# Kernel optimization log

Measured on AMD Instinct MI355X. Metric: run time of the kernel, lower is better.

## Reference

```python
import jax, jax.numpy as jnp
import numpy as np

D_IN = 4096
FEATURES = 4096
BATCH = 4096
NUM_ACTIVE = 50
ACTIVE_VAL = 3.0


def _sparse_init(key, shape, num_active=NUM_ACTIVE, active_val=ACTIVE_VAL):
    # Per output column: num_active inputs start ON (active_val), rest OFF (-3.0)
    scores = jax.random.uniform(key, shape)
    k = min(num_active, shape[0])
    threshold = jnp.sort(scores, axis=0)[-k]
    return jnp.where(scores >= threshold[None, :], active_val, -3.0).astype(jnp.float32)


def setup_inputs() -> dict:
    key = jax.random.key(0)
    kx, kw = jax.random.split(key)
    x = jax.random.normal(kx, (BATCH, D_IN), dtype=jnp.float32)
    w_raw = _sparse_init(kw, (D_IN, FEATURES))
    return {"x": x, "w_raw": w_raw}


def reference(x, w_raw):
    # Binary weights via straight-through estimator.
    w_soft = jax.nn.sigmoid(w_raw)
    w_hard = (w_raw > 0.0).astype(jnp.float32)
    w = w_soft + jax.lax.stop_gradient(w_hard - w_soft)
    return x @ w
```

## Files before the change

### kernel.cpp

```cpp
#include <hip/hip_runtime.h>
#include <hip/hip_fp16.h>

#define D_IN 4096
#define FEAT 4096
#define BATCH 4096
#define MAX_SLOTS 64
#define BFEAT 16
#define RCAP 8
#define OVCAP 16

typedef _Float16 h2 __attribute__((ext_vector_type(2)));

__device__ __forceinline__ h2 bc(unsigned u) { return __builtin_bit_cast(h2, u); }

__global__ void scan_kernel(const float* __restrict__ w,
                            unsigned int* __restrict__ c16,
                            unsigned char* __restrict__ rbuf,
                            unsigned int* __restrict__ ocnt,
                            unsigned short* __restrict__ ovf) {
    int t = blockIdx.x * blockDim.x + threadIdx.x;
    float4 v = ((const float4*)w)[t];
    int flat = t * 4;
    float a[4] = {v.x, v.y, v.z, v.w};
#pragma unroll
    for (int c = 0; c < 4; ++c) {
        if (a[c] > 0.0f) {
            int e = flat + c;
            int F = e & (FEAT - 1);
            int i = e >> 12;
            int r = i & 15;
            unsigned int p = atomicAdd(&c16[(F << 4) + r], 1u);
            if (p < RCAP) {
                rbuf[(size_t)((F << 4) + r) * RCAP + p] = (unsigned char)(i >> 4);
            } else {
                unsigned int op = atomicAdd(&ocnt[F], 1u);
                if (op < OVCAP) ovf[(size_t)F * OVCAP + op] = (unsigned short)i;
            }
        }
    }
}

__global__ __launch_bounds__(256)
void emit_kernel(const unsigned int* __restrict__ c16,
                 const unsigned char* __restrict__ rbuf,
                 const unsigned int* __restrict__ ocnt,
                 const unsigned short* __restrict__ ovf,
                 unsigned int* __restrict__ cnt,
                 unsigned short* __restrict__ idx) {
    __shared__ __align__(16) unsigned short outl[BFEAT][MAX_SLOTS];
    __shared__ unsigned short extras[BFEAT][48];
    __shared__ unsigned char  gapsl[BFEAT][48];
    __shared__ int            scnt[BFEAT][16];
    __shared__ unsigned char  kk[BFEAT][16];
    __shared__ unsigned char  mm[BFEAT][16];
    __shared__ unsigned int   ecnt[BFEAT], gcnt[BFEAT];
    __shared__ unsigned short nn[BFEAT];

    const int tid = threadIdx.x;
    const int f0  = blockIdx.x * BFEAT;
    const int f   = tid >> 4, r = tid & 15;
    const int F   = f0 + f;

    if (tid < BFEAT) { ecnt[tid] = 0u; gcnt[tid] = 0u; }
    ((unsigned int*)outl)[tid] = 0u;
    ((unsigned int*)outl)[tid + 256] = 0u;

    {
        unsigned int c = c16[(F << 4) + r];
        int kr = c > RCAP ? RCAP : (int)c;
        kk[f][r] = (unsigned char)kr;
        scnt[f][r] = kr;
    }
    __syncthreads();

    if (r == 0) {
        int s = 0;
#pragma unroll
        for (int q = 0; q < 16; ++q) s += (int)kk[f][q];
        int ov = (int)ocnt[F]; if (ov > OVCAP) ov = OVCAP;
        s += ov;
        if (s > MAX_SLOTS) s = MAX_SLOTS;
        nn[f] = (unsigned short)s;
        cnt[F] = (unsigned int)s;
    }
    __syncthreads();

    {
        const int n  = (int)nn[f];
        const int kr = (int)kk[f][r];
        uint2 braw = *reinterpret_cast<const uint2*>(rbuf + (size_t)((F << 4) + r) * RCAP);
        const unsigned char* bs = reinterpret_cast<const unsigned char*>(&braw);
        const int base = (r - F) & 15;
        const int tgt  = (n >> 4) + (base < (n & 15) ? 1 : 0);
        const int m    = kr < tgt ? kr : tgt;
        mm[f][r] = (unsigned char)m;
        for (int j = 0; j < m; ++j)
            outl[f][base + (j << 4)] = (unsigned short)(((int)bs[j] << 8) | (r << 4));
    }
    __syncthreads();

    if (tid < MAX_SLOTS) {
        const int p = tid;
        const int j = p >> 4;
        unsigned used = 0u;
        unsigned gapf = 0u;
#pragma unroll
        for (int ff = 0; ff < BFEAT; ++ff) {
            if (p < (int)nn[ff]) {
                const int rr = (p + f0 + ff) & 15;
                if (j < (int)mm[ff][rr]) used |= 1u << rr;
                else                     gapf |= 1u << ff;
            }
        }
        while (gapf) {
            const int ff = __builtin_ctz(gapf);
            gapf &= gapf - 1;
            const int rr = (p + f0 + ff) & 15;
            int got = -1, gr = -1;
            for (int dr = 1; dr < 16; ++dr) {
                const int rc = (rr + dr) & 15;
                if ((used >> rc) & 1u) continue;
                const int t = atomicSub(&scnt[ff][rc], 1) - 1;
                if (t >= (int)mm[ff][rc]) { got = t; gr = rc; break; }
            }
            if (got >= 0) {
                const unsigned char item =
                    rbuf[(size_t)(((f0 + ff) << 4) + gr) * RCAP + got];
                outl[ff][p] = (unsigned short)(((int)item << 8) | (gr << 4));
                used |= 1u << gr;
            } else {
                unsigned int g = atomicAdd(&gcnt[ff], 1u);
                if (g < 48) gapsl[ff][g] = (unsigned char)p;
            }
        }
    }
    __syncthreads();

    {
        const int lo = (int)mm[f][r];
        int hi = scnt[f][r];
        const int kr = (int)kk[f][r];
        if (hi > kr) hi = kr;
        for (int t = lo; t < hi; ++t) {
            unsigned int e = atomicAdd(&ecnt[f], 1u);
            if (e < 48) {
                const unsigned char item = rbuf[(size_t)((F << 4) + r) * RCAP + t];
                extras[f][e] = (unsigned short)(((int)item << 8) | (r << 4));
            }
        }
    }
    if (r == 0) {
        int ov = (int)ocnt[F]; if (ov > OVCAP) ov = OVCAP;
        for (int jj = 0; jj < ov; ++jj) {
            unsigned int e = atomicAdd(&ecnt[f], 1u);
            if (e < 48) extras[f][e] = (unsigned short)(ovf[(size_t)F * OVCAP + jj] << 4);
        }
    }
    __syncthreads();

    if (tid < BFEAT) {
        const int ff = tid;
        int g = (int)gcnt[ff]; if (g > 48) g = 48;
        int e = (int)ecnt[ff]; if (e > 48) e = 48;
        const int m2 = g < e ? g : e;
        for (int t = 0; t < m2; ++t)
            outl[ff][gapsl[ff][t]] = extras[ff][t];
    }
    __syncthreads();

    if (tid < BFEAT * 8) {
        const int ff = tid >> 3, o = tid & 7;
        const uint4 v = *reinterpret_cast<const uint4*>(&outl[ff][o << 3]);
        reinterpret_cast<uint4*>(idx)[(size_t)o * FEAT + f0 + ff] = v;
    }
}

__device__ __forceinline__ void do_oct(uint4 p, const char* __restrict__ xtb,
                                       h2& A01, h2& A23, h2& A45, h2& A67,
                                       h2& B01, h2& B23, h2& B45, h2& B67) {
    uint4 v0 = *(const uint4*)(xtb + (p.x & 0xFFF0u));
    uint4 v1 = *(const uint4*)(xtb + (p.x >> 16));
    uint4 v2 = *(const uint4*)(xtb + (p.y & 0xFFF0u));
    uint4 v3 = *(const uint4*)(xtb + (p.y >> 16));
    uint4 v4 = *(const uint4*)(xtb + (p.z & 0xFFF0u));
    uint4 v5 = *(const uint4*)(xtb + (p.z >> 16));
    uint4 v6 = *(const uint4*)(xtb + (p.w & 0xFFF0u));
    uint4 v7 = *(const uint4*)(xtb + (p.w >> 16));
    A01 += bc(v0.x); A23 += bc(v0.y); A45 += bc(v0.z); A67 += bc(v0.w);
    B01 += bc(v1.x); B23 += bc(v1.y); B45 += bc(v1.z); B67 += bc(v1.w);
    A01 += bc(v2.x); A23 += bc(v2.y); A45 += bc(v2.z); A67 += bc(v2.w);
    B01 += bc(v3.x); B23 += bc(v3.y); B45 += bc(v3.z); B67 += bc(v3.w);
    A01 += bc(v4.x); A23 += bc(v4.y); A45 += bc(v4.z); A67 += bc(v4.w);
    B01 += bc(v5.x); B23 += bc(v5.y); B45 += bc(v5.z); B67 += bc(v5.w);
    A01 += bc(v6.x); A23 += bc(v6.y); A45 += bc(v6.z); A67 += bc(v6.w);
    B01 += bc(v7.x); B23 += bc(v7.y); B45 += bc(v7.z); B67 += bc(v7.w);
}

__global__ __launch_bounds__(1024, 8)
void gather_kernel(const float* __restrict__ x,
                   const unsigned int* __restrict__ cnt,
                   const uint4* __restrict__ q,
                   const unsigned short* __restrict__ q16,
                   float* __restrict__ out) {
    __shared__ uint4 xt[D_IN];
    const int tid = threadIdx.x;
    const int b0  = blockIdx.x * 8;
    const float* xb = x + (size_t)b0 * D_IN;

    {
        const int c4 = tid << 2;
        float4 r0 = *(const float4*)(xb + c4);
        float4 r1 = *(const float4*)(xb + c4 + D_IN);
        float4 r2 = *(const float4*)(xb + c4 + 2 * D_IN);
        float4 r3 = *(const float4*)(xb + c4 + 3 * D_IN);
        float4 r4 = *(const float4*)(xb + c4 + 4 * D_IN);
        float4 r5 = *(const float4*)(xb + c4 + 5 * D_IN);
        float4 r6 = *(const float4*)(xb + c4 + 6 * D_IN);
        float4 r7 = *(const float4*)(xb + c4 + 7 * D_IN);
#define PACK_COL(cc, comp)                                          \
        {                                                           \
            __half2 p01 = __floats2half2_rn(r0.comp, r1.comp);      \
            __half2 p23 = __floats2half2_rn(r2.comp, r3.comp);      \
            __half2 p45 = __floats2half2_rn(r4.comp, r5.comp);      \
            __half2 p67 = __floats2half2_rn(r6.comp, r7.comp);      \
            uint4 v;                                                \
            v.x = *(unsigned*)&p01;                                 \
            v.y = *(unsigned*)&p23;                                 \
            v.z = *(unsigned*)&p45;                                 \
            v.w = *(unsigned*)&p67;                                 \
            xt[c4 + cc] = v;                                        \
        }
        PACK_COL(0, x) PACK_COL(1, y) PACK_COL(2, z) PACK_COL(3, w)
#undef PACK_COL
    }
    __syncthreads();

    const char* xtb = (const char*)xt;

#pragma unroll
    for (int k = 0; k < 4; k += 2) {
        const int fA = tid + k * 1024;
        const int fB = fA + 1024;
        int nA = (int)cnt[fA]; if (nA > MAX_SLOTS) nA = MAX_SLOTS;
        int nB = (int)cnt[fB]; if (nB > MAX_SLOTS) nB = MAX_SLOTS;
        const uint4* qA = q + fA;
        const uint4* qB = q + fB;

        h2 aA01 = {0,0}, aA23 = {0,0}, aA45 = {0,0}, aA67 = {0,0};
        h2 bA01 = {0,0}, bA23 = {0,0}, bA45 = {0,0}, bA67 = {0,0};
        h2 aB01 = {0,0}, aB23 = {0,0}, aB45 = {0,0}, aB67 = {0,0};
        h2 bB01 = {0,0}, bB23 = {0,0}, bB45 = {0,0}, bB67 = {0,0};

        const int nqA = nA >> 3, nqB = nB >> 3;
        const int jm = nqA < nqB ? nqA : nqB;
        if (jm > 0) {
            uint4 pA = qA[0];
            uint4 pB = qB[0];
            for (int j = 0; j < jm; ++j) {
                const int jn = (j + 1 < jm) ? j + 1 : j;
                uint4 nxA = qA[(size_t)jn * FEAT];
                uint4 nxB = qB[(size_t)jn * FEAT];
                do_oct(pA, xtb, aA01, aA23, aA45, aA67, bA01, bA23, bA45, bA67);
                do_oct(pB, xtb, aB01, aB23, aB45, aB67, bB01, bB23, bB45, bB67);
                pA = nxA; pB = nxB;
            }
        }
        for (int j = jm; j < nqA; ++j)
            do_oct(qA[(size_t)j * FEAT], xtb, aA01, aA23, aA45, aA67, bA01, bA23, bA45, bA67);
        for (int j = jm; j < nqB; ++j)
            do_oct(qB[(size_t)j * FEAT], xtb, aB01, aB23, aB45, aB67, bB01, bB23, bB45, bB67);

        {
            int rem = nA & 7;
            int base = (nqA * FEAT + fA) * 8;
            for (int t = 0; t < rem; ++t) {
                uint4 v = *(const uint4*)(xtb + q16[base + t]);
                aA01 += bc(v.x); aA23 += bc(v.y); aA45 += bc(v.z); aA67 += bc(v.w);
            }
        }
        {
            int rem = nB & 7;
            int base = (nqB * FEAT + fB) * 8;
            for (int t = 0; t < rem; ++t) {
                uint4 v = *(const uint4*)(xtb + q16[base + t]);
                aB01 += bc(v.x); aB23 += bc(v.y); aB45 += bc(v.z); aB67 += bc(v.w);
            }
        }

        float* oA = out + fA;
        oA[(size_t)(b0 + 0) * FEAT] = (float)aA01[0] + (float)bA01[0];
        oA[(size_t)(b0 + 1) * FEAT] = (float)aA01[1] + (float)bA01[1];
        oA[(size_t)(b0 + 2) * FEAT] = (float)aA23[0] + (float)bA23[0];
        oA[(size_t)(b0 + 3) * FEAT] = (float)aA23[1] + (float)bA23[1];
        oA[(size_t)(b0 + 4) * FEAT] = (float)aA45[0] + (float)bA45[0];
        oA[(size_t)(b0 + 5) * FEAT] = (float)aA45[1] + (float)bA45[1];
        oA[(size_t)(b0 + 6) * FEAT] = (float)aA67[0] + (float)bA67[0];
        oA[(size_t)(b0 + 7) * FEAT] = (float)aA67[1] + (float)bA67[1];
        float* oB = out + fB;
        oB[(size_t)(b0 + 0) * FEAT] = (float)aB01[0] + (float)bB01[0];
        oB[(size_t)(b0 + 1) * FEAT] = (float)aB01[1] + (float)bB01[1];
        oB[(size_t)(b0 + 2) * FEAT] = (float)aB23[0] + (float)bB23[0];
        oB[(size_t)(b0 + 3) * FEAT] = (float)aB23[1] + (float)bB23[1];
        oB[(size_t)(b0 + 4) * FEAT] = (float)aB45[0] + (float)bB45[0];
        oB[(size_t)(b0 + 5) * FEAT] = (float)aB45[1] + (float)bB45[1];
        oB[(size_t)(b0 + 6) * FEAT] = (float)aB67[0] + (float)bB67[0];
        oB[(size_t)(b0 + 7) * FEAT] = (float)aB67[1] + (float)bB67[1];
    }
}

extern "C" void kernel_launch(void* const* d_in, const int* in_sizes, int n_in,
                              void* d_out, int out_size, void* d_ws, size_t ws_size,
                              hipStream_t stream) {
    const float* x = (const float*)d_in[0];
    const float* w = (const float*)d_in[1];
    float* out = (float*)d_out;

    char* ws = (char*)d_ws;
    unsigned int*   cnt  = (unsigned int*)  (ws);
    unsigned short* idx  = (unsigned short*)(ws + (16u << 10));
    unsigned int*   c16  = (unsigned int*)  (ws + (528u << 10));
    unsigned int*   ocnt = (unsigned int*)  (ws + (784u << 10));
    unsigned char*  rbuf = (unsigned char*) (ws + (800u << 10));
    unsigned short* ovf  = (unsigned short*)(ws + (1312u << 10));

    hipMemsetAsync(c16, 0, (272u << 10), stream);

    scan_kernel<<<(D_IN * FEAT / 4) / 256, 256, 0, stream>>>(w, c16, rbuf, ocnt, ovf);
    emit_kernel<<<FEAT / BFEAT, 256, 0, stream>>>(c16, rbuf, ocnt, ovf, cnt, idx);

    gather_kernel<<<BATCH / 8, 1024, 0, stream>>>(x, cnt, (const uint4*)idx, idx, out);
}
```

Measured before the change: 234.9 us.

## Sort features by nonzero count per block to balance gather wavefront work

In the emit kernel, features within each 16-feature block are sorted by active count and a permutation map (fmap) is written, with the direction alternating every 64 blocks. The gather kernel reads fmap so that adjacent threads in a wavefront process features with similar loop trip counts, which reduces divergence and idle lanes. The bank-rotation offset in emit now uses the sorted slot instead of the feature index, so LDS/bank spreading changes too. It adds a serial insertion sort on one thread per block and one extra indirection load per feature in gather.

```diff
diff --git a/kernel.cpp b/kernel.cpp
--- a/kernel.cpp
+++ b/kernel.cpp
@@ -46,7 +46,8 @@
                  const unsigned int* __restrict__ ocnt,
                  const unsigned short* __restrict__ ovf,
                  unsigned int* __restrict__ cnt,
-                 unsigned short* __restrict__ idx) {
+                 unsigned short* __restrict__ idx,
+                 unsigned short* __restrict__ fmap) {
     __shared__ __align__(16) unsigned short outl[BFEAT][MAX_SLOTS];
     __shared__ unsigned short extras[BFEAT][48];
     __shared__ unsigned char  gapsl[BFEAT][48];
@@ -55,6 +56,7 @@
     __shared__ unsigned char  mm[BFEAT][16];
     __shared__ unsigned int   ecnt[BFEAT], gcnt[BFEAT];
     __shared__ unsigned short nn[BFEAT];
+    __shared__ unsigned char  slotf[BFEAT];
 
     const int tid = threadIdx.x;
     const int f0  = blockIdx.x * BFEAT;
@@ -85,12 +87,30 @@
     }
     __syncthreads();
 
+    if (tid == 0) {
+        unsigned char ord[BFEAT];
+        for (int i = 0; i < BFEAT; ++i) {
+            int j = i;
+            unsigned char cur = (unsigned char)i;
+            while (j > 0 && nn[cur] < nn[ord[j - 1]]) { ord[j] = ord[j - 1]; --j; }
+            ord[j] = cur;
+        }
+        const int wdir = (int)((blockIdx.x >> 6) & 1);
+        for (int s = 0; s < BFEAT; ++s) {
+            const int fl = (int)ord[wdir ? (15 - s) : s];
+            slotf[fl] = (unsigned char)s;
+            fmap[f0 + s] = (unsigned short)(f0 + fl);
+        }
+    }
+    __syncthreads();
+
     {
+        const int sf = (int)slotf[f];
         const int n  = (int)nn[f];
         const int kr = (int)kk[f][r];
         uint2 braw = *reinterpret_cast<const uint2*>(rbuf + (size_t)((F << 4) + r) * RCAP);
         const unsigned char* bs = reinterpret_cast<const unsigned char*>(&braw);
-        const int base = (r - F) & 15;
+        const int base = (r - sf) & 15;
         const int tgt  = (n >> 4) + (base < (n & 15) ? 1 : 0);
         const int m    = kr < tgt ? kr : tgt;
         mm[f][r] = (unsigned char)m;
@@ -107,7 +127,7 @@
 #pragma unroll
         for (int ff = 0; ff < BFEAT; ++ff) {
             if (p < (int)nn[ff]) {
-                const int rr = (p + f0 + ff) & 15;
+                const int rr = (p + (int)slotf[ff]) & 15;
                 if (j < (int)mm[ff][rr]) used |= 1u << rr;
                 else                     gapf |= 1u << ff;
             }
@@ -115,7 +135,7 @@
         while (gapf) {
             const int ff = __builtin_ctz(gapf);
             gapf &= gapf - 1;
-            const int rr = (p + f0 + ff) & 15;
+            const int rr = (p + (int)slotf[ff]) & 15;
             int got = -1, gr = -1;
             for (int dr = 1; dr < 16; ++dr) {
                 const int rc = (rr + dr) & 15;
@@ -201,6 +221,7 @@
                    const unsigned int* __restrict__ cnt,
                    const uint4* __restrict__ q,
                    const unsigned short* __restrict__ q16,
+                   const unsigned short* __restrict__ fmap,
                    float* __restrict__ out) {
     __shared__ uint4 xt[D_IN];
     const int tid = threadIdx.x;
@@ -239,8 +260,8 @@
 
 #pragma unroll
     for (int k = 0; k < 4; k += 2) {
-        const int fA = tid + k * 1024;
-        const int fB = fA + 1024;
+        const int fA = (int)fmap[tid + k * 1024];
+        const int fB = (int)fmap[tid + k * 1024 + 1024];
         int nA = (int)cnt[fA]; if (nA > MAX_SLOTS) nA = MAX_SLOTS;
         int nB = (int)cnt[fB]; if (nB > MAX_SLOTS) nB = MAX_SLOTS;
         const uint4* qA = q + fA;
@@ -322,11 +343,12 @@
     unsigned int*   ocnt = (unsigned int*)  (ws + (784u << 10));
     unsigned char*  rbuf = (unsigned char*) (ws + (800u << 10));
     unsigned short* ovf  = (unsigned short*)(ws + (1312u << 10));
+    unsigned short* fmap = (unsigned short*)(ws + (1440u << 10));
 
     hipMemsetAsync(c16, 0, (272u << 10), stream);
 
     scan_kernel<<<(D_IN * FEAT / 4) / 256, 256, 0, stream>>>(w, c16, rbuf, ocnt, ovf);
-    emit_kernel<<<FEAT / BFEAT, 256, 0, stream>>>(c16, rbuf, ocnt, ovf, cnt, idx);
-
-    gather_kernel<<<BATCH / 8, 1024, 0, stream>>>(x, cnt, (const uint4*)idx, idx, out);
-}
+    emit_kernel<<<FEAT / BFEAT, 256, 0, stream>>>(c16, rbuf, ocnt, ovf, cnt, idx, fmap);
+
+    gather_kernel<<<BATCH / 8, 1024, 0, stream>>>(x, cnt, (const uint4*)idx, idx, fmap, out);
+}
```

New measurement: 239.8 us. 2.1% more time.
